# Optimization experiments

Hardware: AMD Instinct MI355X
Metric: run time of the kernel (lower is better)

## Reference

```python
import jax, jax.numpy as jnp
import numpy as np

HEADS = 8


def setup_inputs() -> dict:
    key = jax.random.key(0)
    ks = jax.random.split(key, 6)
    b, n, dim = 8, 4096, 512
    s = 0.02
    return {
        "x": jax.random.normal(ks[0], (b, n, dim), jnp.float32),
        "Wq": jax.random.normal(ks[1], (dim, dim), jnp.float32) * s,
        "Wk": jax.random.normal(ks[2], (dim, dim), jnp.float32) * s,
        "Wv": jax.random.normal(ks[3], (dim, dim), jnp.float32) * s,
        "Wo": jax.random.normal(ks[4], (dim, dim), jnp.float32) * s,
        "bo": jnp.zeros((dim,), jnp.float32),
    }


def reference(x, Wq, Wk, Wv, Wo, bo):
    b, n, dim = x.shape
    heads = HEADS
    d = dim // heads
    g = int(np.sqrt(n))  # square grid, n chosen as perfect square (no padding)
    scale = d ** -0.5

    def proj(W):
        # [b, n, dim] -> [b, heads, g, g, d]
        t = jnp.einsum('bne,ef->bnf', x, W)
        return t.reshape(b, g, g, heads, d).transpose(0, 3, 1, 2, 4)

    q, k, v = proj(Wq), proj(Wk), proj(Wv)

    # row-wise attention: attend along last grid axis for each row i
    dots_row = jnp.einsum('bnijd,bnikd->bnijk', q, k) * scale
    out_row = jnp.einsum('bnijk,bnikd->bnijd', jax.nn.softmax(dots_row, axis=-1), v)

    # column-wise attention (as in source: transpose grid axes, same einsum pattern)
    q_c, k_c, v_c = (t.swapaxes(2, 3) for t in (q, k, v))
    dots_col = jnp.einsum('bnjid,bnkid->bnjik', q_c, k_c) * scale
    out_col = jnp.einsum('bnjik,bnkid->bnjid', jax.nn.softmax(dots_col, axis=-1), v_c)

    out = out_row + out_col.swapaxes(2, 3)  # [b, heads, g, g, d]
    out = out.transpose(0, 2, 3, 1, 4).reshape(b, n, dim)
    return jnp.einsum('bne,ef->bnf', out, Wo) + bo
```

## Files before the change

### kernel.cpp

```cpp
#include <hip/hip_runtime.h>
#include <hip/hip_bf16.h>
#include <stdint.h>


typedef __bf16 bf16_t;
typedef __bf16 bf16x4v __attribute__((ext_vector_type(4)));
typedef __bf16 bf16x8 __attribute__((ext_vector_type(8)));
typedef float  f32x4  __attribute__((ext_vector_type(4)));

#define GLD16(gp, lp)                                                                  \
  __builtin_amdgcn_global_load_lds((__attribute__((address_space(1))) const void*)(gp),\
                                   (__attribute__((address_space(3))) void*)(lp),      \
                                   16, 0, 0)

__device__ __forceinline__ float  bf2f(bf16_t x) { return (float)x; }
__device__ __forceinline__ bf16_t f2bf(float x)  { return (bf16_t)x; }

__global__ __launch_bounds__(256) void cvt_x(const float* __restrict__ X,
                                             bf16_t* __restrict__ Y, int n4)
{
  int i = blockIdx.x * blockDim.x + threadIdx.x;
  if (i < n4) {
    float4 v = ((const float4*)X)[i];
    bf16x4v o;
    o[0] = f2bf(v.x); o[1] = f2bf(v.y); o[2] = f2bf(v.z); o[3] = f2bf(v.w);
    ((bf16x4v*)Y)[i] = o;
  }
}

__global__ void wt_kernel(const float* __restrict__ Wq, const float* __restrict__ Wk,
                          const float* __restrict__ Wv, const float* __restrict__ Wo,
                          bf16_t* __restrict__ WT)
{
  __shared__ bf16_t tile[32][33];
  const int mat = blockIdx.z;
  const float* W = (mat == 0) ? Wq : (mat == 1) ? Wk : (mat == 2) ? Wv : Wo;
  bf16_t* dst = WT + (size_t)mat * 262144;
  const int tx = threadIdx.x, ty = threadIdx.y;
  const int x0 = blockIdx.x * 32, y0 = blockIdx.y * 32;
#pragma unroll
  for (int i = 0; i < 32; i += 8)
    tile[ty + i][tx] = f2bf(W[(size_t)(y0 + ty + i) * 512 + x0 + tx]);
  __syncthreads();
#pragma unroll
  for (int i = 0; i < 32; i += 8)
    dst[(size_t)(x0 + ty + i) * 512 + y0 + tx] = tile[tx][ty + i];
}

template <bool STORE_F32>
__global__ __launch_bounds__(512, 2) void gemm256(
    const bf16_t* __restrict__ A,
    const bf16_t* __restrict__ BT,
    void* __restrict__ Cp,
    const float* __restrict__ bias,
    int Nd)
{
  __shared__ __align__(16) bf16_t smem[65536];
  bf16_t* const sA = smem;
  bf16_t* const sB = smem + 32768;

  const int tid  = threadIdx.x;
  const int lane = tid & 63, w = tid >> 6;
  const int quad = lane >> 4, r16 = lane & 15;
  const int wr = w >> 2, wc = w & 3;
  const int wm = wr * 128, wn = wc * 64;

  const int G = gridDim.x;
  const int l = blockIdx.y * G + blockIdx.x;
  const int xcd = l & 7, slot = l >> 3;
  const int mb = xcd * (gridDim.y >> 3) + slot / G;
  const int nb = slot % G;
  const int m0 = mb * 256, n0 = nb * 256;

  const int srow = tid >> 3;
  const int sseg = (tid & 7) ^ (srow & 7);
  const bf16_t* Ag = A  + (size_t)(m0 + srow) * 512 + sseg * 8;
  const bf16_t* Bg = BT + (size_t)(n0 + srow) * 512 + sseg * 8;
  const bf16_t *AgC[4], *BgC[4];
#pragma unroll
  for (int c = 0; c < 4; ++c) {
    AgC[c] = Ag + (size_t)c * 32768;
    BgC[c] = Bg + (size_t)c * 32768;
  }
  const int sdst = w * 512;

  GLD16(BgC[0], sB + sdst);
  GLD16(BgC[1], sB + 4096  + sdst);
  GLD16(BgC[2], sB + 8192  + sdst);
  GLD16(BgC[3], sB + 12288 + sdst);
  GLD16(AgC[0], sA + sdst);
  GLD16(AgC[2], sA + 8192  + sdst);
  GLD16(AgC[1], sA + 4096  + sdst);
  GLD16(AgC[3], sA + 12288 + sdst);

  f32x4 acc[8][4] = {};

  const int xsw   = (r16 & 7) << 4;
  const int koff0 = (quad * 16) ^ xsw;
  const int koff1 = (64 + quad * 16) ^ xsw;

#pragma unroll
  for (int t = 0; t < 8; ++t) {
    const int p = t & 1, pn = p ^ 1;
    const int kn = (t + 1) * 64;
    const char* sAp = (const char*)(sA + p * 16384);
    const char* sBp = (const char*)(sB + p * 16384);
    bf16_t* const dA = sA + pn * 16384 + sdst;
    bf16_t* const dB = sB + pn * 16384 + sdst;
    bf16x8 a0[4], a1[4], b0[4], b1[4];

    asm volatile("s_waitcnt vmcnt(2)" ::: "memory");
    __builtin_amdgcn_s_barrier();
    asm volatile("" ::: "memory");
#pragma unroll
    for (int i = 0; i < 4; ++i) {
      a0[i] = *(const bf16x8*)(sAp + (size_t)(wm + i * 16 + r16) * 128 + koff0);
      a1[i] = *(const bf16x8*)(sAp + (size_t)(wm + i * 16 + r16) * 128 + koff1);
    }
#pragma unroll
    for (int j = 0; j < 4; ++j) {
      b0[j] = *(const bf16x8*)(sBp + (size_t)(wn + j * 16 + r16) * 128 + koff0);
      b1[j] = *(const bf16x8*)(sBp + (size_t)(wn + j * 16 + r16) * 128 + koff1);
    }
    GLD16(BgC[0] + kn, dB);
    GLD16(BgC[1] + kn, dB + 4096);
    GLD16(BgC[2] + kn, dB + 8192);
    GLD16(BgC[3] + kn, dB + 12288);
    __builtin_amdgcn_s_setprio(1);
#pragma unroll
    for (int i = 0; i < 4; ++i)
#pragma unroll
      for (int j = 0; j < 4; ++j)
        acc[i][j] = __builtin_amdgcn_mfma_f32_16x16x32_bf16(a0[i], b0[j], acc[i][j], 0, 0, 0);
#pragma unroll
    for (int i = 0; i < 4; ++i)
#pragma unroll
      for (int j = 0; j < 4; ++j)
        acc[i][j] = __builtin_amdgcn_mfma_f32_16x16x32_bf16(a1[i], b1[j], acc[i][j], 0, 0, 0);
    __builtin_amdgcn_s_setprio(0);

    asm volatile("s_waitcnt vmcnt(4)" ::: "memory");
    __builtin_amdgcn_s_barrier();
    asm volatile("" ::: "memory");
#pragma unroll
    for (int i = 0; i < 4; ++i) {
      a0[i] = *(const bf16x8*)(sAp + (size_t)(wm + 64 + i * 16 + r16) * 128 + koff0);
      a1[i] = *(const bf16x8*)(sAp + (size_t)(wm + 64 + i * 16 + r16) * 128 + koff1);
    }
    GLD16(AgC[0] + kn, dA);
    GLD16(AgC[2] + kn, dA + 8192);
    GLD16(AgC[1] + kn, dA + 4096);
    GLD16(AgC[3] + kn, dA + 12288);
    __builtin_amdgcn_s_setprio(1);
#pragma unroll
    for (int i = 0; i < 4; ++i)
#pragma unroll
      for (int j = 0; j < 4; ++j)
        acc[4 + i][j] = __builtin_amdgcn_mfma_f32_16x16x32_bf16(a0[i], b0[j], acc[4 + i][j], 0, 0, 0);
#pragma unroll
    for (int i = 0; i < 4; ++i)
#pragma unroll
      for (int j = 0; j < 4; ++j)
        acc[4 + i][j] = __builtin_amdgcn_mfma_f32_16x16x32_bf16(a1[i], b1[j], acc[4 + i][j], 0, 0, 0);
    __builtin_amdgcn_s_setprio(0);
  }

  asm volatile("s_waitcnt vmcnt(0)" ::: "memory");
  __syncthreads();

  if (STORE_F32) {
    float* C = (float*)Cp;
#pragma unroll
    for (int i8 = 0; i8 < 8; ++i8) {
#pragma unroll
      for (int j = 0; j < 4; ++j) {
        const int row = m0 + wm + i8 * 16 + quad * 4;
        const int col = n0 + wn + j * 16 + r16;
        const float bv = bias ? bias[col] : 0.0f;
#pragma unroll
        for (int rg = 0; rg < 4; ++rg)
          C[(size_t)(row + rg) * Nd + col] = acc[i8][j][rg] + bv;
      }
    }
  } else {
    bf16_t* Es = smem;
    bf16_t* C  = (bf16_t*)Cp;
#pragma unroll
    for (int pr = 0; pr < 2; ++pr) {
      if (pr) __syncthreads();
      if (wr == pr) {
#pragma unroll
        for (int i8 = 0; i8 < 8; ++i8)
#pragma unroll
          for (int j = 0; j < 4; ++j)
#pragma unroll
            for (int rg = 0; rg < 4; ++rg)
              Es[(size_t)(i8 * 16 + quad * 4 + rg) * 264 + wn + j * 16 + r16] =
                  f2bf(acc[i8][j][rg]);
      }
      __syncthreads();
#pragma unroll
      for (int ps = 0; ps < 8; ++ps) {
        const int row = ps * 16 + (tid >> 5);
        const int cs  = (tid & 31) * 8;
        *(bf16x8*)&C[(size_t)(m0 + pr * 128 + row) * Nd + n0 + cs] =
            *(const bf16x8*)&Es[(size_t)row * 264 + cs];
      }
    }
  }
}

__global__ __launch_bounds__(256) void cc_attn(
    const bf16_t* __restrict__ QKV, bf16_t* __restrict__ Aout)
{
  __shared__ __align__(16) bf16_t Qs[64 * 72];
  __shared__ __align__(16) bf16_t Ks[64 * 72];
  __shared__ __align__(16) bf16_t VsT[64 * 70];

  const int gidx = blockIdx.x;
  const int r = gidx & 63, h = (gidx >> 6) & 7, b = gidx >> 9;
  const int tid = threadIdx.x, lane = tid & 63, w = tid >> 6;
  const int quad = lane >> 4, r16 = lane & 15;
  const size_t row0 = (size_t)b * 4096 + (size_t)r * 64;

  {
    const int row = tid >> 2, seg = tid & 3;
    const bf16_t* gp = QKV + (row0 + row) * 1536 + h * 64 + seg * 16;
    *(bf16x8*)&Qs[row * 72 + seg * 16]     = *(const bf16x8*)&gp[0];
    *(bf16x8*)&Qs[row * 72 + seg * 16 + 8] = *(const bf16x8*)&gp[8];
    *(bf16x8*)&Ks[row * 72 + seg * 16]     = *(const bf16x8*)&gp[512];
    *(bf16x8*)&Ks[row * 72 + seg * 16 + 8] = *(const bf16x8*)&gp[520];
    bf16x8 v0 = *(const bf16x8*)&gp[1024];
    bf16x8 v1 = *(const bf16x8*)&gp[1032];
#pragma unroll
    for (int e = 0; e < 8; ++e) {
      VsT[(seg * 16 + e) * 70 + row]     = v0[e];
      VsT[(seg * 16 + 8 + e) * 70 + row] = v1[e];
    }
  }
  __syncthreads();

  f32x4 sacc[4] = {};
#pragma unroll
  for (int ks = 0; ks < 2; ++ks) {
    bf16x8 aq = *(const bf16x8*)&Qs[(w * 16 + r16) * 72 + ks * 32 + quad * 8];
#pragma unroll
    for (int nj = 0; nj < 4; ++nj) {
      bf16x8 bk = *(const bf16x8*)&Ks[(nj * 16 + r16) * 72 + ks * 32 + quad * 8];
      sacc[nj] = __builtin_amdgcn_mfma_f32_16x16x32_bf16(aq, bk, sacc[nj], 0, 0, 0);
    }
  }

  float ex[4][4];
  float sm[4];
#pragma unroll
  for (int rg = 0; rg < 4; ++rg) {
    float m = -3.0e38f;
#pragma unroll
    for (int nj = 0; nj < 4; ++nj) {
      ex[nj][rg] = sacc[nj][rg] * 0.125f;
      m = fmaxf(m, ex[nj][rg]);
    }
    m = fmaxf(m, __shfl_xor(m, 1));
    m = fmaxf(m, __shfl_xor(m, 2));
    m = fmaxf(m, __shfl_xor(m, 4));
    m = fmaxf(m, __shfl_xor(m, 8));
    float s = 0.f;
#pragma unroll
    for (int nj = 0; nj < 4; ++nj) { ex[nj][rg] = __expf(ex[nj][rg] - m); s += ex[nj][rg]; }
    s += __shfl_xor(s, 1);
    s += __shfl_xor(s, 2);
    s += __shfl_xor(s, 4);
    s += __shfl_xor(s, 8);
    sm[rg] = 2.0f / s;
  }

  __syncthreads();
#pragma unroll
  for (int nj = 0; nj < 4; ++nj)
#pragma unroll
    for (int rg = 0; rg < 4; ++rg)
      Qs[(w * 16 + quad * 4 + rg) * 72 + nj * 16 + r16] = f2bf(ex[nj][rg] * sm[rg]);
  __syncthreads();

  f32x4 oacc[4] = {};
#pragma unroll
  for (int ks = 0; ks < 2; ++ks) {
    bf16x8 ap = *(const bf16x8*)&Qs[(w * 16 + r16) * 72 + ks * 32 + quad * 8];
#pragma unroll
    for (int nj = 0; nj < 4; ++nj) {
      bf16x8 bv = *(const bf16x8*)&VsT[(nj * 16 + r16) * 70 + ks * 32 + quad * 8];
      oacc[nj] = __builtin_amdgcn_mfma_f32_16x16x32_bf16(ap, bv, oacc[nj], 0, 0, 0);
    }
  }

  {
    bf16_t* Es = Ks;
#pragma unroll
    for (int nj = 0; nj < 4; ++nj)
#pragma unroll
      for (int rg = 0; rg < 4; ++rg)
        Es[(w * 16 + quad * 4 + rg) * 72 + nj * 16 + r16] = f2bf(oacc[nj][rg]);
    __syncthreads();
    const size_t obase = row0 * 512 + (size_t)h * 64;
#pragma unroll
    for (int rd = 0; rd < 2; ++rd) {
      const int row = rd * 32 + (tid >> 3);
      const int col = (tid & 7) * 8;
      *(bf16x8*)&Aout[obase + (size_t)row * 512 + col] = *(const bf16x8*)&Es[row * 72 + col];
    }
  }
}

extern "C" void kernel_launch(void* const* d_in, const int* in_sizes, int n_in,
                              void* d_out, int out_size, void* d_ws, size_t ws_size,
                              hipStream_t stream)
{
  const float* x  = (const float*)d_in[0];
  const float* Wq = (const float*)d_in[1];
  const float* Wk = (const float*)d_in[2];
  const float* Wv = (const float*)d_in[3];
  const float* Wo = (const float*)d_in[4];
  const float* bo = (const float*)d_in[5];

  bf16_t* ws = (bf16_t*)d_ws;
  bf16_t* WT  = ws;
  bf16_t* xbf = ws + 1048576;
  bf16_t* QKV = xbf + 16777216;
  bf16_t* Ab  = xbf;

  cvt_x<<<dim3(16384), 256, 0, stream>>>(x, xbf, 4194304);
  wt_kernel<<<dim3(16, 16, 4), dim3(32, 8), 0, stream>>>(Wq, Wk, Wv, Wo, WT);

  gemm256<false><<<dim3(6, 128), 512, 0, stream>>>(xbf, WT, QKV, nullptr, 1536);

  cc_attn<<<dim3(4096), 256, 0, stream>>>(QKV, Ab);

  gemm256<true><<<dim3(2, 128), 512, 0, stream>>>(Ab, WT + 786432, d_out, bo, 512);
}
```

Baseline: 234.1 us.

## Restructure GEMM main loop into fine-grained LDS-read/MFMA software pipeline

Result: no change. 232.4 us (-0.7%).

```diff
diff --git a/kernel.cpp b/kernel.cpp
--- a/kernel.cpp
+++ b/kernel.cpp
@@ -76,22 +76,16 @@
   const int sseg = (tid & 7) ^ (srow & 7);
   const bf16_t* Ag = A  + (size_t)(m0 + srow) * 512 + sseg * 8;
   const bf16_t* Bg = BT + (size_t)(n0 + srow) * 512 + sseg * 8;
-  const bf16_t *AgC[4], *BgC[4];
-#pragma unroll
-  for (int c = 0; c < 4; ++c) {
-    AgC[c] = Ag + (size_t)c * 32768;
-    BgC[c] = Bg + (size_t)c * 32768;
-  }
   const int sdst = w * 512;
 
-  GLD16(BgC[0], sB + sdst);
-  GLD16(BgC[1], sB + 4096  + sdst);
-  GLD16(BgC[2], sB + 8192  + sdst);
-  GLD16(BgC[3], sB + 12288 + sdst);
-  GLD16(AgC[0], sA + sdst);
-  GLD16(AgC[2], sA + 8192  + sdst);
-  GLD16(AgC[1], sA + 4096  + sdst);
-  GLD16(AgC[3], sA + 12288 + sdst);
+  GLD16(Bg,           sB + sdst);
+  GLD16(Bg + 32768,   sB + 4096  + sdst);
+  GLD16(Bg + 65536,   sB + 8192  + sdst);
+  GLD16(Bg + 98304,   sB + 12288 + sdst);
+  GLD16(Ag,           sA + sdst);
+  GLD16(Ag + 32768,   sA + 4096  + sdst);
+  GLD16(Ag + 65536,   sA + 8192  + sdst);
+  GLD16(Ag + 98304,   sA + 12288 + sdst);
 
   f32x4 acc[8][4] = {};
 
@@ -99,73 +93,81 @@
   const int koff0 = (quad * 16) ^ xsw;
   const int koff1 = (64 + quad * 16) ^ xsw;
 
+  bf16x8 bk[2][4];
+  bf16x8 a[2][2];
+
+#define RD_B(dst, base, kof)                                                     \
+  _Pragma("unroll") for (int j_ = 0; j_ < 4; ++j_)                               \
+    dst[j_] = *(const bf16x8*)((base) + (size_t)(wn + j_ * 16 + r16) * 128 + (kof));
+#define RD_A2(dst, base, rowoff, kof)                                            \
+  _Pragma("unroll") for (int i_ = 0; i_ < 2; ++i_)                               \
+    dst[i_] = *(const bf16x8*)((base) + (size_t)(wm + (rowoff) + i_ * 16 + r16) * 128 + (kof));
+#define MFMA8(r0, r1, av, bv)                                                    \
+  __builtin_amdgcn_s_setprio(1);                                                 \
+  _Pragma("unroll") for (int j_ = 0; j_ < 4; ++j_) {                             \
+    acc[r0][j_] = __builtin_amdgcn_mfma_f32_16x16x32_bf16(av[0], bv[j_], acc[r0][j_], 0, 0, 0); \
+    acc[r1][j_] = __builtin_amdgcn_mfma_f32_16x16x32_bf16(av[1], bv[j_], acc[r1][j_], 0, 0, 0); \
+  }                                                                              \
+  __builtin_amdgcn_s_setprio(0);
+
+  asm volatile("s_waitcnt vmcnt(0)" ::: "memory");
+  __builtin_amdgcn_s_barrier();
+
+  RD_B(bk[0], (const char*)sB, koff0);
+  RD_A2(a[0], (const char*)sA, 0, koff0);
+
 #pragma unroll
   for (int t = 0; t < 8; ++t) {
     const int p = t & 1, pn = p ^ 1;
-    const int kn = (t + 1) * 64;
-    const char* sAp = (const char*)(sA + p * 16384);
-    const char* sBp = (const char*)(sB + p * 16384);
-    bf16_t* const dA = sA + pn * 16384 + sdst;
-    bf16_t* const dB = sB + pn * 16384 + sdst;
-    bf16x8 a0[4], a1[4], b0[4], b1[4];
-
-    asm volatile("s_waitcnt vmcnt(2)" ::: "memory");
-    __builtin_amdgcn_s_barrier();
-    asm volatile("" ::: "memory");
-#pragma unroll
-    for (int i = 0; i < 4; ++i) {
-      a0[i] = *(const bf16x8*)(sAp + (size_t)(wm + i * 16 + r16) * 128 + koff0);
-      a1[i] = *(const bf16x8*)(sAp + (size_t)(wm + i * 16 + r16) * 128 + koff1);
-    }
-#pragma unroll
-    for (int j = 0; j < 4; ++j) {
-      b0[j] = *(const bf16x8*)(sBp + (size_t)(wn + j * 16 + r16) * 128 + koff0);
-      b1[j] = *(const bf16x8*)(sBp + (size_t)(wn + j * 16 + r16) * 128 + koff1);
-    }
-    GLD16(BgC[0] + kn, dB);
-    GLD16(BgC[1] + kn, dB + 4096);
-    GLD16(BgC[2] + kn, dB + 8192);
-    GLD16(BgC[3] + kn, dB + 12288);
-    __builtin_amdgcn_s_setprio(1);
-#pragma unroll
-    for (int i = 0; i < 4; ++i)
-#pragma unroll
-      for (int j = 0; j < 4; ++j)
-        acc[i][j] = __builtin_amdgcn_mfma_f32_16x16x32_bf16(a0[i], b0[j], acc[i][j], 0, 0, 0);
-#pragma unroll
-    for (int i = 0; i < 4; ++i)
-#pragma unroll
-      for (int j = 0; j < 4; ++j)
-        acc[i][j] = __builtin_amdgcn_mfma_f32_16x16x32_bf16(a1[i], b1[j], acc[i][j], 0, 0, 0);
-    __builtin_amdgcn_s_setprio(0);
-
-    asm volatile("s_waitcnt vmcnt(4)" ::: "memory");
-    __builtin_amdgcn_s_barrier();
-    asm volatile("" ::: "memory");
-#pragma unroll
-    for (int i = 0; i < 4; ++i) {
-      a0[i] = *(const bf16x8*)(sAp + (size_t)(wm + 64 + i * 16 + r16) * 128 + koff0);
-      a1[i] = *(const bf16x8*)(sAp + (size_t)(wm + 64 + i * 16 + r16) * 128 + koff1);
-    }
-    GLD16(AgC[0] + kn, dA);
-    GLD16(AgC[2] + kn, dA + 8192);
-    GLD16(AgC[1] + kn, dA + 4096);
-    GLD16(AgC[3] + kn, dA + 12288);
-    __builtin_amdgcn_s_setprio(1);
-#pragma unroll
-    for (int i = 0; i < 4; ++i)
-#pragma unroll
-      for (int j = 0; j < 4; ++j)
-        acc[4 + i][j] = __builtin_amdgcn_mfma_f32_16x16x32_bf16(a0[i], b0[j], acc[4 + i][j], 0, 0, 0);
-#pragma unroll
-    for (int i = 0; i < 4; ++i)
-#pragma unroll
-      for (int j = 0; j < 4; ++j)
-        acc[4 + i][j] = __builtin_amdgcn_mfma_f32_16x16x32_bf16(a1[i], b1[j], acc[4 + i][j], 0, 0, 0);
-    __builtin_amdgcn_s_setprio(0);
-  }
-
-  asm volatile("s_waitcnt vmcnt(0)" ::: "memory");
+    const char* sAp  = (const char*)(sA + p  * 16384);
+    const char* sBp  = (const char*)(sB + p  * 16384);
+    const char* sApn = (const char*)(sA + pn * 16384);
+    const char* sBpn = (const char*)(sB + pn * 16384);
+
+    if (t < 7) {
+      const int kn = (t + 1) * 64;
+      bf16_t* const dA = sA + pn * 16384 + sdst;
+      bf16_t* const dB = sB + pn * 16384 + sdst;
+      GLD16(Bg + kn,          dB);
+      GLD16(Bg + kn + 32768,  dB + 4096);
+      GLD16(Bg + kn + 65536,  dB + 8192);
+      GLD16(Bg + kn + 98304,  dB + 12288);
+      GLD16(Ag + kn,          dA);
+      GLD16(Ag + kn + 32768,  dA + 4096);
+      GLD16(Ag + kn + 65536,  dA + 8192);
+      GLD16(Ag + kn + 98304,  dA + 12288);
+    }
+    RD_A2(a[1], sAp, 32, koff0);
+    MFMA8(0, 1, a[0], bk[0]);
+
+    RD_A2(a[0], sAp, 64, koff0);
+    MFMA8(2, 3, a[1], bk[0]);
+
+    RD_A2(a[1], sAp, 96, koff0);
+    MFMA8(4, 5, a[0], bk[0]);
+
+    RD_B(bk[1], sBp, koff1);
+    RD_A2(a[0], sAp, 0, koff1);
+    MFMA8(6, 7, a[1], bk[0]);
+
+    RD_A2(a[1], sAp, 32, koff1);
+    MFMA8(0, 1, a[0], bk[1]);
+
+    RD_A2(a[0], sAp, 64, koff1);
+    MFMA8(2, 3, a[1], bk[1]);
+
+    RD_A2(a[1], sAp, 96, koff1);
+    MFMA8(4, 5, a[0], bk[1]);
+
+    if (t < 7) {
+      asm volatile("s_waitcnt vmcnt(0)" ::: "memory");
+      __builtin_amdgcn_s_barrier();
+      RD_B(bk[0], sBpn, koff0);
+      RD_A2(a[0], sApn, 0, koff0);
+    }
+    MFMA8(6, 7, a[1], bk[1]);
+  }
+
   __syncthreads();
 
   if (STORE_F32) {
@@ -208,6 +210,9 @@
       }
     }
   }
+#undef RD_B
+#undef RD_A2
+#undef MFMA8
 }
 
 __global__ __launch_bounds__(256) void cc_attn(
```
